# Optimization experiments

Hardware: AMD Instinct MI355X
Metric: run time of the kernel (lower is better)

## Reference

```python
import jax, jax.numpy as jnp
import numpy as np

N = 50000      # nodes
E = 250000     # edges
IN = 256       # in_channels
OUT = 256      # out_channels
H = 4          # heads
C = OUT // H   # per-head channels = 64
MSG = 128
TIME = 64
ED = MSG + TIME + 2   # edge_dim = 194


def _glorot(k, shape):
    return (jax.random.normal(k, shape, jnp.float32) / np.sqrt(shape[0])).astype(jnp.float32)


def setup_inputs() -> dict:
    ks = jax.random.split(jax.random.key(0), 16)
    z = lambda: jnp.zeros((H * C,), jnp.float32)
    inp = {
        "x": jax.random.normal(ks[0], (N, IN), jnp.float32),
        "edge_index": jax.random.randint(ks[1], (2, E), 0, N),
        "edge_attr": jax.random.normal(ks[2], (E, ED), jnp.float32),
        # conv1 params (in_channels=IN)
        "Wq1": _glorot(ks[3], (IN, H * C)), "bq1": z(),
        "Wk1": _glorot(ks[4], (IN, H * C)), "bk1": z(),
        "Wv1": _glorot(ks[5], (IN, H * C)), "bv1": z(),
        "We1": _glorot(ks[6], (ED, H * C)),              # lin_edge has no bias in PyG
        "Ws1": _glorot(ks[7], (IN, H * C)), "bs1": z(),  # skip/root connection
        # conv2 params (in_channels=OUT)
        "Wq2": _glorot(ks[8], (OUT, H * C)), "bq2": z(),
        "Wk2": _glorot(ks[9], (OUT, H * C)), "bk2": z(),
        "Wv2": _glorot(ks[10], (OUT, H * C)), "bv2": z(),
        "We2": _glorot(ks[11], (ED, H * C)),
        "Ws2": _glorot(ks[12], (OUT, H * C)), "bs2": z(),
    }
    return inp


def _tconv(x, src, dst, edge_attr, Wq, bq, Wk, bk, Wv, bv, We, Ws, bs):
    """PyG TransformerConv (heads=H, concat=True, root_weight=True), eval mode."""
    n = x.shape[0]
    q = (x @ Wq + bq).reshape(n, H, C)
    k = (x @ Wk + bk).reshape(n, H, C)
    v = (x @ Wv + bv).reshape(n, H, C)
    e = (edge_attr @ We).reshape(-1, H, C)          # [E,H,C]
    kj = k[src] + e                                  # key + edge embedding
    vj = v[src] + e                                  # value + edge embedding
    logits = jnp.einsum('ehc,ehc->eh', q[dst], kj) / np.sqrt(C)  # [E,H]
    # segment softmax over incoming edges of each dst node
    m = jax.lax.stop_gradient(jax.ops.segment_max(logits, dst, num_segments=n))
    ex = jnp.exp(logits - m[dst])
    denom = jax.ops.segment_sum(ex, dst, num_segments=n)
    a = ex / (denom[dst] + 1e-16)                    # [E,H]
    agg = jax.ops.segment_sum(vj * a[:, :, None], dst, num_segments=n)  # [N,H,C]
    return agg.reshape(n, H * C) + x @ Ws + bs


def reference(x, edge_index, edge_attr,
              Wq1, bq1, Wk1, bk1, Wv1, bv1, We1, Ws1, bs1,
              Wq2, bq2, Wk2, bk2, Wv2, bv2, We2, Ws2, bs2):
    src, dst = edge_index[0], edge_index[1]
    h = jax.nn.relu(_tconv(x, src, dst, edge_attr,
                           Wq1, bq1, Wk1, bk1, Wv1, bv1, We1, Ws1, bs1))
    # dropout is identity in eval mode
    return _tconv(h, src, dst, edge_attr,
                  Wq2, bq2, Wk2, bk2, Wv2, bv2, We2, Ws2, bs2)
```

## Files before the change

### kernel.cpp

```cpp
#include <hip/hip_runtime.h>

#define N_NODES 50000
#define N_EDGES 250000
#define DIM 256
#define ED 194
#define EDP 224
#define MP_NODE 50048
#define MP_EDGE 250112

typedef __bf16 bf16x8 __attribute__((ext_vector_type(8)));
typedef float f32x4 __attribute__((ext_vector_type(4)));
typedef short s16x8 __attribute__((ext_vector_type(8)));
typedef short s16x4 __attribute__((ext_vector_type(4)));
typedef unsigned short u16x8 __attribute__((ext_vector_type(8)));

__device__ __forceinline__ float bf2f(unsigned short b){
  union { unsigned int u; float f; } v; v.u = ((unsigned int)b)<<16; return v.f;
}
__device__ __forceinline__ short f2bf(float f){
  union { float f; unsigned int u; } v; v.f = f;
  unsigned int u = v.u;
  return (short)((u + 0x7fffu + ((u>>16)&1u))>>16);
}

__device__ __forceinline__ void gload_lds16(const void* g, void* l){
  __builtin_amdgcn_global_load_lds(
      (const __attribute__((address_space(1))) unsigned int*)g,
      (__attribute__((address_space(3))) unsigned int*)l, 16, 0, 0);
}

__global__ __launch_bounds__(256) void convert_x_kernel(
    const float* __restrict__ x, short* __restrict__ xb)
{
  int idx = blockIdx.x*256 + threadIdx.x;
  s16x4 o;
  if (idx < N_NODES*64){
    float4 a = *(const float4*)(x + (size_t)idx*4);
    o[0]=f2bf(a.x); o[1]=f2bf(a.y); o[2]=f2bf(a.z); o[3]=f2bf(a.w);
  } else {
    o[0]=0; o[1]=0; o[2]=0; o[3]=0;
  }
  *(s16x4*)(xb + (size_t)idx*4) = o;
}

#define E_ROWS 32
__global__ __launch_bounds__(256) void convert_e_kernel(
    const float* __restrict__ ea, short* __restrict__ eb)
{
  __shared__ float lds[E_ROWS*ED];
  int row0 = blockIdx.x * E_ROWS;
  int tid = threadIdx.x;
  int base = row0 * ED;
  int valid = N_EDGES*ED - base;

  for (int i = tid; i < E_ROWS*ED/4; i += 256){
    float4 v;
    if (i*4 < valid) v = *(const float4*)(ea + base + i*4);
    else             v = make_float4(0.f,0.f,0.f,0.f);
    *(float4*)(lds + i*4) = v;
  }
  __syncthreads();

  for (int u = tid; u < E_ROWS*28; u += 256){
    int row = u / 28;
    int c8  = u - row*28;
    int col = c8*8;
    s16x8 o;
    if (col + 8 <= ED){
      #pragma unroll
      for (int j2=0;j2<4;j2++){
        float2 f = *(const float2*)(lds + row*ED + col + j2*2);
        o[j2*2]   = f2bf(f.x);
        o[j2*2+1] = f2bf(f.y);
      }
    } else {
      #pragma unroll
      for (int j=0;j<8;j++){
        int c = col + j;
        o[j] = (c < ED) ? f2bf(lds[row*ED + c]) : (short)0;
      }
    }
    *(s16x8*)(eb + (size_t)(row0+row)*EDP + col) = o;
  }
}

__global__ __launch_bounds__(256) void transpose_node_w(
    const float* __restrict__ Wq, const float* __restrict__ Wk,
    const float* __restrict__ Wv, const float* __restrict__ Ws,
    short* __restrict__ WtN)
{
  int idx = blockIdx.x*256 + threadIdx.x;
  int w = idx>>16, rem = idx&65535;
  int i = rem>>8, o = rem&255;
  const float* W = (w==0)?Wq:((w==1)?Wk:((w==2)?Wv:Ws));
  WtN[(w<<16) + o*256 + i] = f2bf(W[i*256+o]);
}
__global__ __launch_bounds__(256) void bias_cat_kernel(
    const float* __restrict__ b0, const float* __restrict__ b1,
    const float* __restrict__ b2, const float* __restrict__ b3,
    float* __restrict__ biasN)
{
  int t = blockIdx.x*256 + threadIdx.x;
  const float* b = (t<256)?b0:((t<512)?b1:((t<768)?b2:b3));
  biasN[t] = b[t&255];
}
__global__ __launch_bounds__(256) void transpose_edge_w(
    const float* __restrict__ We, short* __restrict__ WtE)
{
  int idx = blockIdx.x*256 + threadIdx.x;
  int k = idx>>8, o = idx&255;
  WtE[o*EDP + k] = (k<ED) ? f2bf(We[k*256+o]) : (short)0;
}

__global__ __launch_bounds__(256) void zero_ints(int* __restrict__ p, int n){
  int i = blockIdx.x*256 + threadIdx.x;
  if (i<n) p[i] = 0;
}
__global__ __launch_bounds__(256) void count_deg(const int* __restrict__ dst, int* __restrict__ deg){
  int e = blockIdx.x*256 + threadIdx.x;
  if (e < N_EDGES) atomicAdd(&deg[dst[e]], 1);
}
#define SCAN_NBLK 196
__global__ __launch_bounds__(256) void scan_p1(const int* __restrict__ deg, int* __restrict__ part){
  int t = threadIdx.x;
  int i = blockIdx.x*256 + t;
  int v = (i<N_NODES)? deg[i] : 0;
  #pragma unroll
  for (int off=32; off; off>>=1) v += __shfl_xor(v, off, 64);
  __shared__ int s[4];
  if ((t&63)==0) s[t>>6] = v;
  __syncthreads();
  if (t==0) part[blockIdx.x] = s[0]+s[1]+s[2]+s[3];
}
__global__ __launch_bounds__(256) void scan_p2(int* __restrict__ part){
  __shared__ int s[256];
  int t = threadIdx.x;
  int v = (t<SCAN_NBLK)? part[t] : 0;
  s[t] = v; __syncthreads();
  for (int off=1; off<256; off<<=1){
    int x = (t>=off)? s[t-off] : 0;
    __syncthreads();
    s[t] += x;
    __syncthreads();
  }
  part[t] = (t==0)? 0 : s[t-1];
}
__global__ __launch_bounds__(256) void scan_p3(const int* __restrict__ deg,
    const int* __restrict__ part, int* __restrict__ rowptr, int* __restrict__ cursor){
  __shared__ int s[256];
  int t = threadIdx.x;
  int i = blockIdx.x*256 + t;
  int v = (i<N_NODES)? deg[i] : 0;
  s[t] = v; __syncthreads();
  for (int off=1; off<256; off<<=1){
    int x = (t>=off)? s[t-off] : 0;
    __syncthreads();
    s[t] += x;
    __syncthreads();
  }
  if (i < N_NODES){ rowptr[i+1] = part[blockIdx.x] + s[t]; cursor[i] = 0; }
  if (i == 0) rowptr[0] = 0;
}
__global__ __launch_bounds__(256) void scatter_edges(
    const int* __restrict__ src, const int* __restrict__ dst,
    const int* __restrict__ rowptr, int* __restrict__ cursor, int2* __restrict__ csr)
{
  int e = blockIdx.x*256 + threadIdx.x;
  if (e < N_EDGES){
    int d = dst[e];
    int pos = atomicAdd(&cursor[d], 1);
    csr[rowptr[d] + pos] = make_int2(src[e]<<11, e<<9);
  }
}

template<int K, int NLD, bool HAS_BIAS>
__global__ __launch_bounds__(256) void gemm_bt(
    const short* __restrict__ A, const short* __restrict__ Bt,
    const float* __restrict__ bias, short* __restrict__ out, int M)
{
  __shared__ short As[128*32];
  __shared__ short Bs[128*32];
  int tid = threadIdx.x;
  int lane = tid & 63, wave = tid >> 6;
  int m0 = blockIdx.x*128, n0 = blockIdx.y*128;

  int srow = tid>>2, scol = (tid&3)*8;
  const short* gA = A + (size_t)(m0+srow)*K + scol;
  const short* gB = Bt + (size_t)(n0+srow)*K + scol;
  short* ldsA1 = As + wave*512;
  short* ldsA2 = As + 2048 + wave*512;
  short* ldsB1 = Bs + wave*512;
  short* ldsB2 = Bs + 2048 + wave*512;

  int wr = wave>>1, wc = wave&1;
  int fr = lane & 15;
  int kq = lane >> 4;
  f32x4 acc[4][4];
  #pragma unroll
  for (int a=0;a<4;a++)
    #pragma unroll
    for (int b=0;b<4;b++) acc[a][b] = (f32x4){0.f,0.f,0.f,0.f};

  for (int k0=0; k0<K; k0+=32){
    __syncthreads();
    gload_lds16(gA + k0,                ldsA1);
    gload_lds16(gA + (size_t)64*K + k0, ldsA2);
    gload_lds16(gB + k0,                ldsB1);
    gload_lds16(gB + (size_t)64*K + k0, ldsB2);
    __syncthreads();

    bf16x8 af[4], bf[4];
    const short* ar = As + (wr*64 + fr)*32 + kq*8;
    const short* br = Bs + (wc*64 + fr)*32 + kq*8;
    #pragma unroll
    for (int fm=0;fm<4;fm++) af[fm] = *(const bf16x8*)(ar + fm*512);
    #pragma unroll
    for (int fn=0;fn<4;fn++) bf[fn] = *(const bf16x8*)(br + fn*512);
    #pragma unroll
    for (int fm=0;fm<4;fm++)
      #pragma unroll
      for (int fn=0;fn<4;fn++)
        acc[fm][fn] = __builtin_amdgcn_mfma_f32_16x16x32_bf16(af[fm], bf[fn], acc[fm][fn], 0, 0, 0);
  }

  int cr = (lane>>4)*4;
  int cc = lane & 15;
  #pragma unroll
  for (int fm=0;fm<4;fm++){
    #pragma unroll
    for (int fn=0;fn<4;fn++){
      int col = n0 + wc*64 + fn*16 + cc;
      float bv = HAS_BIAS ? bias[col] : 0.f;
      #pragma unroll
      for (int i=0;i<4;i++){
        int row = m0 + wr*64 + fm*16 + cr + i;
        if (row < M) out[(size_t)row*NLD + col] = f2bf(acc[fm][fn][i] + bv);
      }
    }
  }
}

__global__ __launch_bounds__(256) void edge_phase_kernel(
    const short* __restrict__ QKVS, const short* __restrict__ Eemb,
    const int* __restrict__ rowptr, const int2* __restrict__ csr,
    short* __restrict__ out_bf, float* __restrict__ out_f, int relu)
{
  int tid = threadIdx.x, wave = tid>>6, lane = tid&63;
  int node = blockIdx.x*4 + wave;
  if (node >= N_NODES){
    if (node < MP_NODE && out_bf){
      s16x4 z; z[0]=0; z[1]=0; z[2]=0; z[3]=0;
      *(s16x4*)(out_bf + (size_t)node*256 + lane*4) = z;
    }
    return;
  }
  int half = lane>>5;
  int hl   = lane&31;
  int c8   = hl*8;
  const unsigned short* base = (const unsigned short*)QKVS + (size_t)node*1024;

  u16x8 qu = *(const u16x8*)(base + c8);
  float q[8];
  #pragma unroll
  for (int j=0;j<8;j++) q[j] = bf2f(qu[j])*0.125f;

  int beg = rowptr[node], end = rowptr[node+1];
  float l = 0.f;
  float a[8];
  #pragma unroll
  for (int j=0;j<8;j++) a[j] = 0.f;
  int kb = 512 + hl*16;
  int ebo = hl*16;

  for (int idx = beg; idx < end; idx += 2){
    int j = idx + half;
    int jc = (j < end) ? j : (end-1);
    int2 se = csr[jc];
    const char* Kp = (const char*)QKVS + (unsigned)(se.x + kb);
    const char* Ep = (const char*)Eemb + (unsigned)(se.y + ebo);
    u16x8 ku = *(const u16x8*)Kp;
    u16x8 vu = *(const u16x8*)(Kp + 512);
    u16x8 eu = *(const u16x8*)Ep;
    float vv[8];
    float t = 0.f;
    #pragma unroll
    for (int c=0;c<8;c++){
      float ef = bf2f(eu[c]);
      float kf = bf2f(ku[c]) + ef;
      vv[c]    = bf2f(vu[c]) + ef;
      t += q[c]*kf;
    }
    t += __shfl_xor(t, 1, 64);
    t += __shfl_xor(t, 2, 64);
    t += __shfl_xor(t, 4, 64);
    float p = (j < end) ? __expf(t) : 0.f;
    l += p;
    #pragma unroll
    for (int c=0;c<8;c++) a[c] += p*vv[c];
  }

  l += __shfl_xor(l, 32, 64);
  #pragma unroll
  for (int c=0;c<8;c++) a[c] += __shfl_xor(a[c], 32, 64);

  float inv = (l > 0.f) ? 1.0f/l : 0.f;
  u16x8 su = *(const u16x8*)(base + 768 + c8);
  float r[8];
  #pragma unroll
  for (int c=0;c<8;c++){
    float v = a[c]*inv + bf2f(su[c]);
    r[c] = relu ? fmaxf(v, 0.f) : v;
  }

  if (out_bf){
    if (!half){
      s16x8 o;
      #pragma unroll
      for (int c=0;c<8;c++) o[c] = f2bf(r[c]);
      *(s16x8*)(out_bf + (size_t)node*256 + c8) = o;
    }
  } else {
    float4 st = half ? make_float4(r[4],r[5],r[6],r[7])
                     : make_float4(r[0],r[1],r[2],r[3]);
    *(float4*)(out_f + (size_t)node*256 + c8 + half*4) = st;
  }
}

extern "C" void kernel_launch(void* const* d_in, const int* in_sizes, int n_in,
                              void* d_out, int out_size, void* d_ws, size_t ws_size,
                              hipStream_t stream)
{
  const float* x     = (const float*)d_in[0];
  const int*   eidx  = (const int*)d_in[1];
  const float* eattr = (const float*)d_in[2];
  const float* Wq1=(const float*)d_in[3],  *bq1=(const float*)d_in[4];
  const float* Wk1=(const float*)d_in[5],  *bk1=(const float*)d_in[6];
  const float* Wv1=(const float*)d_in[7],  *bv1=(const float*)d_in[8];
  const float* We1=(const float*)d_in[9];
  const float* Ws1=(const float*)d_in[10], *bs1=(const float*)d_in[11];
  const float* Wq2=(const float*)d_in[12], *bq2=(const float*)d_in[13];
  const float* Wk2=(const float*)d_in[14], *bk2=(const float*)d_in[15];
  const float* Wv2=(const float*)d_in[16], *bv2=(const float*)d_in[17];
  const float* We2=(const float*)d_in[18];
  const float* Ws2=(const float*)d_in[19], *bs2=(const float*)d_in[20];

  char* ws = (char*)d_ws;
  size_t off = 0;
  auto alloc = [&](size_t bytes)->char*{
    char* p = ws + off; off = (off + bytes + 255) & ~(size_t)255; return p;
  };
  short* QKVS  = (short*)alloc((size_t)N_NODES*1024*2);
  short* Eemb  = (short*)alloc((size_t)N_EDGES*256*2);
  short* x_bf  = (short*)alloc((size_t)MP_NODE*DIM*2);
  short* h_bf  = (short*)alloc((size_t)MP_NODE*DIM*2);
  short* e_bf  = (short*)alloc((size_t)MP_EDGE*EDP*2);
  short* WtN   = (short*)alloc((size_t)4*65536*2);
  short* WtE   = (short*)alloc((size_t)256*EDP*2);
  float* biasN = (float*)alloc((size_t)1024*4);
  int*   deg   = (int*)alloc((size_t)N_NODES*4);
  int*   rowptr= (int*)alloc((size_t)(N_NODES+1)*4);
  int*   cursor= (int*)alloc((size_t)N_NODES*4);
  int*   part  = (int*)alloc((size_t)256*4);
  int2*  csr   = (int2*)alloc((size_t)N_EDGES*8);

  const int* srcp = eidx;
  const int* dstp = eidx + N_EDGES;

  const int EB = (N_EDGES + 255)/256;
  const int NB = (N_NODES + 255)/256;

  convert_x_kernel<<<MP_NODE*64/256,256,0,stream>>>(x, x_bf);
  convert_e_kernel<<<MP_EDGE/E_ROWS,256,0,stream>>>(eattr, e_bf);

  zero_ints<<<NB,256,0,stream>>>(deg, N_NODES);
  count_deg<<<EB,256,0,stream>>>(dstp, deg);
  scan_p1<<<SCAN_NBLK,256,0,stream>>>(deg, part);
  scan_p2<<<1,256,0,stream>>>(part);
  scan_p3<<<SCAN_NBLK,256,0,stream>>>(deg, part, rowptr, cursor);
  scatter_edges<<<EB,256,0,stream>>>(srcp, dstp, rowptr, cursor, csr);

  transpose_node_w<<<1024,256,0,stream>>>(Wq1,Wk1,Wv1,Ws1,WtN);
  bias_cat_kernel<<<4,256,0,stream>>>(bq1,bk1,bv1,bs1,biasN);
  transpose_edge_w<<<224,256,0,stream>>>(We1,WtE);
  gemm_bt<DIM,1024,true><<<dim3(MP_NODE/128,8),256,0,stream>>>(x_bf, WtN, biasN, QKVS, N_NODES);
  gemm_bt<EDP,256,false><<<dim3(MP_EDGE/128,2),256,0,stream>>>(e_bf, WtE, nullptr, Eemb, N_EDGES);
  edge_phase_kernel<<<MP_NODE/4,256,0,stream>>>(QKVS,Eemb,rowptr,csr,h_bf,nullptr,1);

  transpose_node_w<<<1024,256,0,stream>>>(Wq2,Wk2,Wv2,Ws2,WtN);
  bias_cat_kernel<<<4,256,0,stream>>>(bq2,bk2,bv2,bs2,biasN);
  transpose_edge_w<<<224,256,0,stream>>>(We2,WtE);
  gemm_bt<DIM,1024,true><<<dim3(MP_NODE/128,8),256,0,stream>>>(h_bf, WtN, biasN, QKVS, N_NODES);
  gemm_bt<EDP,256,false><<<dim3(MP_EDGE/128,2),256,0,stream>>>(e_bf, WtE, nullptr, Eemb, N_EDGES);
  edge_phase_kernel<<<N_NODES/4,256,0,stream>>>(QKVS,Eemb,rowptr,csr,nullptr,(float*)d_out,0);
}
```

Measured before the change: 877.6 us.

## Store edge embeddings in CSR order via permuted gather in edge GEMM

The edge-embedding GEMM now gathers its input rows through a dst-sorted edge permutation, so Eemb is written in CSR order. The edge-phase kernel can then read edge embeddings sequentially by CSR index instead of randomly by original edge id, and the CSR entries shrink from int2 to int. The cost is scattered row gathers of the edge-attribute input inside the GEMM loads, plus a padded Eemb allocation.

```diff
diff --git a/kernel.cpp b/kernel.cpp
--- a/kernel.cpp
+++ b/kernel.cpp
@@ -163,20 +163,24 @@
 }
 __global__ __launch_bounds__(256) void scatter_edges(
     const int* __restrict__ src, const int* __restrict__ dst,
-    const int* __restrict__ rowptr, int* __restrict__ cursor, int2* __restrict__ csr)
+    const int* __restrict__ rowptr, int* __restrict__ cursor,
+    int* __restrict__ csrx, int* __restrict__ eperm)
 {
   int e = blockIdx.x*256 + threadIdx.x;
   if (e < N_EDGES){
     int d = dst[e];
     int pos = atomicAdd(&cursor[d], 1);
-    csr[rowptr[d] + pos] = make_int2(src[e]<<11, e<<9);
-  }
-}
-
-template<int K, int NLD, bool HAS_BIAS>
+    int p = rowptr[d] + pos;
+    csrx[p] = src[e]<<11;
+    eperm[p] = e;
+  }
+}
+
+template<int K, int NLD, bool HAS_BIAS, bool PERM>
 __global__ __launch_bounds__(256) void gemm_bt(
     const short* __restrict__ A, const short* __restrict__ Bt,
-    const float* __restrict__ bias, short* __restrict__ out, int M)
+    const float* __restrict__ bias, short* __restrict__ out, int M,
+    const int* __restrict__ perm)
 {
   __shared__ short As[128*32];
   __shared__ short Bs[128*32];
@@ -185,7 +189,12 @@
   int m0 = blockIdx.x*128, n0 = blockIdx.y*128;
 
   int srow = tid>>2, scol = (tid&3)*8;
-  const short* gA = A + (size_t)(m0+srow)*K + scol;
+  int arow = m0 + srow;
+  if (PERM) arow = (arow < M) ? perm[arow] : 0;
+  int arow2 = m0 + 64 + srow;
+  if (PERM) arow2 = (arow2 < M) ? perm[arow2] : 0;
+  const short* gA  = A + (size_t)arow*K + scol;
+  const short* gA2 = A + (size_t)arow2*K + scol;
   const short* gB = Bt + (size_t)(n0+srow)*K + scol;
   short* ldsA1 = As + wave*512;
   short* ldsA2 = As + 2048 + wave*512;
@@ -203,8 +212,8 @@
 
   for (int k0=0; k0<K; k0+=32){
     __syncthreads();
-    gload_lds16(gA + k0,                ldsA1);
-    gload_lds16(gA + (size_t)64*K + k0, ldsA2);
+    gload_lds16(gA + k0,  ldsA1);
+    gload_lds16(PERM ? (gA2 + k0) : (gA + (size_t)64*K + k0), ldsA2);
     gload_lds16(gB + k0,                ldsB1);
     gload_lds16(gB + (size_t)64*K + k0, ldsB2);
     __syncthreads();
@@ -242,7 +251,7 @@
 
 __global__ __launch_bounds__(256) void edge_phase_kernel(
     const short* __restrict__ QKVS, const short* __restrict__ Eemb,
-    const int* __restrict__ rowptr, const int2* __restrict__ csr,
+    const int* __restrict__ rowptr, const int* __restrict__ csrx,
     short* __restrict__ out_bf, float* __restrict__ out_f, int relu)
 {
   int tid = threadIdx.x, wave = tid>>6, lane = tid&63;
@@ -275,12 +284,12 @@
   for (int idx = beg; idx < end; idx += 2){
     int j = idx + half;
     int jc = (j < end) ? j : (end-1);
-    int2 se = csr[jc];
-    const char* Kp = (const char*)QKVS + (unsigned)(se.x + kb);
-    const char* Ep = (const char*)Eemb + (unsigned)(se.y + ebo);
+    int sx = csrx[jc];
+    const char* Ep = (const char*)Eemb + ((unsigned)(jc<<9) + ebo);
+    const char* Kp = (const char*)QKVS + (unsigned)(sx + kb);
+    u16x8 eu = *(const u16x8*)Ep;
     u16x8 ku = *(const u16x8*)Kp;
     u16x8 vu = *(const u16x8*)(Kp + 512);
-    u16x8 eu = *(const u16x8*)Ep;
     float vv[8];
     float t = 0.f;
     #pragma unroll
@@ -350,7 +359,7 @@
     char* p = ws + off; off = (off + bytes + 255) & ~(size_t)255; return p;
   };
   short* QKVS  = (short*)alloc((size_t)N_NODES*1024*2);
-  short* Eemb  = (short*)alloc((size_t)N_EDGES*256*2);
+  short* Eemb  = (short*)alloc((size_t)MP_EDGE*256*2);
   short* x_bf  = (short*)alloc((size_t)MP_NODE*DIM*2);
   short* h_bf  = (short*)alloc((size_t)MP_NODE*DIM*2);
   short* e_bf  = (short*)alloc((size_t)MP_EDGE*EDP*2);
@@ -361,7 +370,8 @@
   int*   rowptr= (int*)alloc((size_t)(N_NODES+1)*4);
   int*   cursor= (int*)alloc((size_t)N_NODES*4);
   int*   part  = (int*)alloc((size_t)256*4);
-  int2*  csr   = (int2*)alloc((size_t)N_EDGES*8);
+  int*   csrx  = (int*)alloc((size_t)N_EDGES*4);
+  int*   eperm = (int*)alloc((size_t)N_EDGES*4);
 
   const int* srcp = eidx;
   const int* dstp = eidx + N_EDGES;
@@ -377,19 +387,19 @@
   scan_p1<<<SCAN_NBLK,256,0,stream>>>(deg, part);
   scan_p2<<<1,256,0,stream>>>(part);
   scan_p3<<<SCAN_NBLK,256,0,stream>>>(deg, part, rowptr, cursor);
-  scatter_edges<<<EB,256,0,stream>>>(srcp, dstp, rowptr, cursor, csr);
+  scatter_edges<<<EB,256,0,stream>>>(srcp, dstp, rowptr, cursor, csrx, eperm);
 
   transpose_node_w<<<1024,256,0,stream>>>(Wq1,Wk1,Wv1,Ws1,WtN);
   bias_cat_kernel<<<4,256,0,stream>>>(bq1,bk1,bv1,bs1,biasN);
   transpose_edge_w<<<224,256,0,stream>>>(We1,WtE);
-  gemm_bt<DIM,1024,true><<<dim3(MP_NODE/128,8),256,0,stream>>>(x_bf, WtN, biasN, QKVS, N_NODES);
-  gemm_bt<EDP,256,false><<<dim3(MP_EDGE/128,2),256,0,stream>>>(e_bf, WtE, nullptr, Eemb, N_EDGES);
-  edge_phase_kernel<<<MP_NODE/4,256,0,stream>>>(QKVS,Eemb,rowptr,csr,h_bf,nullptr,1);
+  gemm_bt<DIM,1024,true,false><<<dim3(MP_NODE/128,8),256,0,stream>>>(x_bf, WtN, biasN, QKVS, N_NODES, nullptr);
+  gemm_bt<EDP,256,false,true><<<dim3(MP_EDGE/128,2),256,0,stream>>>(e_bf, WtE, nullptr, Eemb, N_EDGES, eperm);
+  edge_phase_kernel<<<MP_NODE/4,256,0,stream>>>(QKVS,Eemb,rowptr,csrx,h_bf,nullptr,1);
 
   transpose_node_w<<<1024,256,0,stream>>>(Wq2,Wk2,Wv2,Ws2,WtN);
   bias_cat_kernel<<<4,256,0,stream>>>(bq2,bk2,bv2,bs2,biasN);
   transpose_edge_w<<<224,256,0,stream>>>(We2,WtE);
-  gemm_bt<DIM,1024,true><<<dim3(MP_NODE/128,8),256,0,stream>>>(h_bf, WtN, biasN, QKVS, N_NODES);
-  gemm_bt<EDP,256,false><<<dim3(MP_EDGE/128,2),256,0,stream>>>(e_bf, WtE, nullptr, Eemb, N_EDGES);
-  edge_phase_kernel<<<N_NODES/4,256,0,stream>>>(QKVS,Eemb,rowptr,csr,nullptr,(float*)d_out,0);
-}
+  gemm_bt<DIM,1024,true,false><<<dim3(MP_NODE/128,8),256,0,stream>>>(h_bf, WtN, biasN, QKVS, N_NODES, nullptr);
+  gemm_bt<EDP,256,false,true><<<dim3(MP_EDGE/128,2),256,0,stream>>>(e_bf, WtE, nullptr, Eemb, N_EDGES, eperm);
+  edge_phase_kernel<<<N_NODES/4,256,0,stream>>>(QKVS,Eemb,rowptr,csrx,nullptr,(float*)d_out,0);
+}
```

Result: no change. 887.9 us (+1.2%).
